# Optimization experiments

Hardware: AMD Instinct MI355X
Metric: run time of the kernel (lower is better)

The kernel has to match this reference:

```python
import jax, jax.numpy as jnp
import numpy as np

HEAD_NUM = 16
KEY_DIM = 64
EMBED = 1024
KV_OUT = HEAD_NUM * KEY_DIM  # 1024


def setup_inputs() -> dict:
    key = jax.random.key(0)
    ks = jax.random.split(key, 11)
    B, L, E = 2, 2048, EMBED
    scale = 0.02
    return {
        "query": jax.random.normal(ks[0], (B, L, E), jnp.float32),
        "key": jax.random.normal(ks[1], (B, L, E), jnp.float32),
        "value": jax.random.normal(ks[2], (B, L, E), jnp.float32),
        "W_Query": jax.random.normal(ks[3], (E, KV_OUT), jnp.float32) * scale,
        "W_Key": jax.random.normal(ks[4], (E, KV_OUT), jnp.float32) * scale,
        "W_Value": jax.random.normal(ks[5], (E, KV_OUT), jnp.float32) * scale,
        "W_Output": jax.random.normal(ks[6], (KV_OUT, E), jnp.float32) * scale,
        "B_Query": jnp.zeros((KV_OUT,), jnp.float32),
        "B_Key": jnp.zeros((KV_OUT,), jnp.float32),
        "B_Value": jnp.zeros((KV_OUT,), jnp.float32),
        "B_Output": jnp.zeros((E,), jnp.float32),
    }


def reference(query, key, value, W_Query, W_Key, W_Value, W_Output,
              B_Query, B_Key, B_Value, B_Output):
    B, Lq, E = query.shape
    Lk = key.shape[1]
    H, D = HEAD_NUM, KEY_DIM
    # QKV projections + bias
    q = query @ W_Query + B_Query            # [B, Lq, H*D]
    k = key @ W_Key + B_Key                  # [B, Lk, H*D]
    v = value @ W_Value + B_Value            # [B, Lk, H*D]
    # tf.split(axis=2) per head == reshape to [B, L, H, D]
    q = q.reshape(B, Lq, H, D)
    k = k.reshape(B, Lk, H, D)
    v = v.reshape(B, Lk, H, D)
    # scaled dot-product attention (no mask, dropout=0)
    scores = jnp.einsum("bqhd,bkhd->bhqk", q, k) / (D ** 0.5)
    probs = jax.nn.softmax(scores, axis=-1)
    out = jnp.einsum("bhqk,bkhd->bqhd", probs, v)  # [B, Lq, H, D]
    out = out.reshape(B, Lq, H * D)
    return out @ W_Output + B_Output
```

## Files before the change

### kernel.cpp

```cpp
#include <hip/hip_runtime.h>

using u16 = unsigned short;
using u32 = unsigned int;

typedef __attribute__((ext_vector_type(8))) short bf16x8;
typedef __attribute__((ext_vector_type(4))) float f32x4;
typedef __attribute__((ext_vector_type(4))) u32 u32x4;
typedef __attribute__((ext_vector_type(2))) u32 u32x2;
typedef __attribute__((ext_vector_type(4))) _Float16 f16x4;

#define MFMA_BF16_K32(a, b, c) __builtin_amdgcn_mfma_f32_16x16x32_bf16((a), (b), (c), 0, 0, 0)
#define MFMA_F16_K16(a, b, c) __builtin_amdgcn_mfma_f32_16x16x16f16((a), (b), (c), 0, 0, 0)

#define QSCALE 0.18033688011112042f

extern "C" __device__ float __ocml_native_exp2_f32(float);

__device__ __forceinline__ u16 f2bf(float f) {
  u32 u = __builtin_bit_cast(u32, f);
  return (u16)((u + 0x7fffu + ((u >> 16) & 1u)) >> 16);
}

__device__ __forceinline__ u32 pk_f16(float a, float b) {
  auto v = __builtin_amdgcn_cvt_pkrtz(a, b);
  return __builtin_bit_cast(u32, v);
}

__device__ __forceinline__ void load_lds16(const void* g, void* l) {
  __builtin_amdgcn_global_load_lds((__attribute__((address_space(1))) void*)g,
                                   (__attribute__((address_space(3))) void*)l,
                                   16, 0, 0);
}

__global__ __launch_bounds__(256) void cvt_all_kernel(
    const float* __restrict__ q, const float* __restrict__ k, const float* __restrict__ v,
    u16* __restrict__ oq, u16* __restrict__ ok, u16* __restrict__ ov,
    const float* __restrict__ w0, const float* __restrict__ w1,
    const float* __restrict__ w2, const float* __restrict__ w3,
    u16* __restrict__ d0, u16* __restrict__ d1,
    u16* __restrict__ d2, u16* __restrict__ d3) {
  const int id = blockIdx.x;
  const int tid = threadIdx.x;
  if (id < 6144) {
    const int z = id >> 11, bx = id & 2047;
    const float* s = z == 0 ? q : z == 1 ? k : v;
    u16* d = z == 0 ? oq : z == 1 ? ok : ov;
    int i = (bx * 256 + tid) * 8;
    f32x4 a = *(const f32x4*)(s + i);
    f32x4 b = *(const f32x4*)(s + i + 4);
    u32x4 o;
    o.x = (u32)f2bf(a.x) | ((u32)f2bf(a.y) << 16);
    o.y = (u32)f2bf(a.z) | ((u32)f2bf(a.w) << 16);
    o.z = (u32)f2bf(b.x) | ((u32)f2bf(b.y) << 16);
    o.w = (u32)f2bf(b.z) | ((u32)f2bf(b.w) << 16);
    *(u32x4*)(d + i) = o;
    return;
  }
  __shared__ float t[64][65];
  const int r0 = id - 6144;
  const int z = r0 >> 8, rr0 = r0 & 255;
  const int bx = rr0 & 15, by = rr0 >> 4;
  const float* src = z == 0 ? w0 : z == 1 ? w1 : z == 2 ? w2 : w3;
  u16* dst = z == 0 ? d0 : z == 1 ? d1 : z == 2 ? d2 : d3;
  const float scale = (z == 0) ? QSCALE : 1.0f;
  const int r = tid >> 4, c4 = (tid & 15) * 4;
#pragma unroll
  for (int i = 0; i < 4; ++i) {
    int row = r + i * 16;
    f32x4 vv = *(const f32x4*)(src + (by * 64 + row) * 1024 + bx * 64 + c4);
    t[row][c4 + 0] = vv.x;
    t[row][c4 + 1] = vv.y;
    t[row][c4 + 2] = vv.z;
    t[row][c4 + 3] = vv.w;
  }
  __syncthreads();
  const int rw = tid >> 2, cc = (tid & 3) * 16;
  alignas(16) u16 tmp[16];
#pragma unroll
  for (int j = 0; j < 16; ++j) tmp[j] = f2bf(t[cc + j][rw] * scale);
  u32x4* outp = (u32x4*)(dst + (bx * 64 + rw) * 1024 + by * 64 + cc);
  outp[0] = *(const u32x4*)&tmp[0];
  outp[1] = *(const u32x4*)&tmp[8];
}

__global__ __launch_bounds__(256) void gemm_qkv_kernel(
    const u16* __restrict__ x0, const u16* __restrict__ x1, const u16* __restrict__ x2,
    const u16* __restrict__ w0, const u16* __restrict__ w1, const u16* __restrict__ w2,
    const float* __restrict__ b0, const float* __restrict__ b1, const float* __restrict__ b2,
    u16* __restrict__ c0, u16* __restrict__ c1, u16* __restrict__ vt) {
  __shared__ u16 As[128 * 64];
  __shared__ u16 Bs[128 * 64];
  const int lid = blockIdx.x;
  const int xcd = lid & 7, rr = lid >> 3;
  const int nb = rr & 7, slot = rr >> 3;
  const int g = slot * 8 + xcd;
  const int z = g >> 5, m_idx = g & 31;
  const u16* A = z == 0 ? x0 : z == 1 ? x1 : x2;
  const u16* Bt = z == 0 ? w0 : z == 1 ? w1 : w2;
  const float* bias = z == 0 ? b0 : z == 1 ? b1 : b2;
  const float bscale = z == 0 ? QSCALE : 1.0f;
  const int tid = threadIdx.x;
  const int wave = tid >> 6, lane = tid & 63;
  const int l16 = lane & 15, quad = lane >> 4;
  const int l7 = l16 & 7;
  const int wm = wave >> 1, wn = wave & 1;
  const int m0 = m_idx * 128, n0 = nb * 128;

  f32x4 acc[4][4];
  const f32x4 zf = {0.f, 0.f, 0.f, 0.f};
#pragma unroll
  for (int i = 0; i < 4; ++i)
#pragma unroll
    for (int j = 0; j < 4; ++j) acc[i][j] = zf;

  for (int kb = 0; kb < 1024; kb += 64) {
#pragma unroll
    for (int t = 0; t < 4; ++t) {
      int c = wave * 256 + t * 64 + lane;
      int row = c >> 3, sc8 = (c & 7) ^ (row & 7);
      load_lds16(A + (m0 + row) * 1024 + kb + sc8 * 8, &As[(wave * 256 + t * 64) * 8]);
    }
#pragma unroll
    for (int t = 0; t < 4; ++t) {
      int c = wave * 256 + t * 64 + lane;
      int row = c >> 3, sc8 = (c & 7) ^ (row & 7);
      load_lds16(Bt + (n0 + row) * 1024 + kb + sc8 * 8, &Bs[(wave * 256 + t * 64) * 8]);
    }
    asm volatile("s_waitcnt vmcnt(0)" ::: "memory");
    __syncthreads();
#pragma unroll
    for (int ks = 0; ks < 2; ++ks) {
      const int sch = (ks * 4 + quad) ^ l7;
      bf16x8 af[4], bfv[4];
#pragma unroll
      for (int mt = 0; mt < 4; ++mt)
        af[mt] = *(const bf16x8*)&As[(wm * 64 + mt * 16 + l16) * 64 + sch * 8];
#pragma unroll
      for (int nt = 0; nt < 4; ++nt)
        bfv[nt] = *(const bf16x8*)&Bs[(wn * 64 + nt * 16 + l16) * 64 + sch * 8];
#pragma unroll
      for (int mt = 0; mt < 4; ++mt)
#pragma unroll
        for (int nt = 0; nt < 4; ++nt) acc[mt][nt] = MFMA_BF16_K32(af[mt], bfv[nt], acc[mt][nt]);
    }
    __syncthreads();
  }

  float bv[4];
#pragma unroll
  for (int nt = 0; nt < 4; ++nt) bv[nt] = bias[n0 + wn * 64 + nt * 16 + l16] * bscale;
  if (z != 2) {
    u16* C = z == 0 ? c0 : c1;
#pragma unroll
    for (int mt = 0; mt < 4; ++mt)
#pragma unroll
      for (int nt = 0; nt < 4; ++nt)
#pragma unroll
        for (int r = 0; r < 4; ++r) {
          int row = m0 + wm * 64 + mt * 16 + quad * 4 + r;
          int col = n0 + wn * 64 + nt * 16 + l16;
          C[row * 1024 + col] = f2bf(acc[mt][nt][r] + bv[nt]);
        }
  } else {
#pragma unroll
    for (int mt = 0; mt < 4; ++mt)
#pragma unroll
      for (int nt = 0; nt < 4; ++nt)
#pragma unroll
        for (int r = 0; r < 4; ++r) {
          int row = m0 + wm * 64 + mt * 16 + quad * 4 + r;
          int col = n0 + wn * 64 + nt * 16 + l16;
          int bb = row >> 11, kv = row & 2047;
          _Float16 hv = (_Float16)(acc[mt][nt][r] + bv[nt]);
          vt[(bb * 1024 + col) * 2048 + kv] = __builtin_bit_cast(u16, hv);
        }
  }
}

__global__ __launch_bounds__(256) void gemm_out_kernel(const u16* __restrict__ A,
                                                       const u16* __restrict__ Bt,
                                                       const float* __restrict__ bias,
                                                       float* __restrict__ C) {
  __shared__ u16 As[64 * 64];
  __shared__ u16 Bs[128 * 64];
  const int lid = blockIdx.x;
  const int xcd = lid & 7, rr = lid >> 3;
  const int nb = rr & 7, slot = rr >> 3;
  const int by = slot * 8 + xcd;
  const int tid = threadIdx.x;
  const int wave = tid >> 6, lane = tid & 63;
  const int l16 = lane & 15, quad = lane >> 4;
  const int l7 = l16 & 7;
  const int m0 = by * 64, n0 = nb * 128;

  f32x4 acc[4][2];
  const f32x4 zf = {0.f, 0.f, 0.f, 0.f};
#pragma unroll
  for (int i = 0; i < 4; ++i)
#pragma unroll
    for (int j = 0; j < 2; ++j) acc[i][j] = zf;

  for (int kb = 0; kb < 1024; kb += 64) {
#pragma unroll
    for (int t = 0; t < 2; ++t) {
      int c = wave * 128 + t * 64 + lane;
      int row = c >> 3, sc8 = (c & 7) ^ (row & 7);
      load_lds16(A + (m0 + row) * 1024 + kb + sc8 * 8, &As[(wave * 128 + t * 64) * 8]);
    }
#pragma unroll
    for (int t = 0; t < 4; ++t) {
      int c = wave * 256 + t * 64 + lane;
      int row = c >> 3, sc8 = (c & 7) ^ (row & 7);
      load_lds16(Bt + (n0 + row) * 1024 + kb + sc8 * 8, &Bs[(wave * 256 + t * 64) * 8]);
    }
    asm volatile("s_waitcnt vmcnt(0)" ::: "memory");
    __syncthreads();
#pragma unroll
    for (int ks = 0; ks < 2; ++ks) {
      const int sch = (ks * 4 + quad) ^ l7;
      bf16x8 af[4], bfv[2];
#pragma unroll
      for (int mt = 0; mt < 4; ++mt)
        af[mt] = *(const bf16x8*)&As[(mt * 16 + l16) * 64 + sch * 8];
#pragma unroll
      for (int nt = 0; nt < 2; ++nt)
        bfv[nt] = *(const bf16x8*)&Bs[(wave * 32 + nt * 16 + l16) * 64 + sch * 8];
#pragma unroll
      for (int mt = 0; mt < 4; ++mt)
#pragma unroll
        for (int nt = 0; nt < 2; ++nt) acc[mt][nt] = MFMA_BF16_K32(af[mt], bfv[nt], acc[mt][nt]);
    }
    __syncthreads();
  }

  float bv[2];
#pragma unroll
  for (int nt = 0; nt < 2; ++nt) bv[nt] = bias[n0 + wave * 32 + nt * 16 + l16];
#pragma unroll
  for (int mt = 0; mt < 4; ++mt)
#pragma unroll
    for (int nt = 0; nt < 2; ++nt)
#pragma unroll
      for (int r = 0; r < 4; ++r) {
        int row = m0 + mt * 16 + quad * 4 + r;
        int col = n0 + wave * 32 + nt * 16 + l16;
        C[row * 1024 + col] = acc[mt][nt][r] + bv[nt];
      }
}

__global__ __launch_bounds__(256, 4) void flash_kernel(const u16* __restrict__ Q,
                                                       const u16* __restrict__ K,
                                                       const u16* __restrict__ Vt,
                                                       u16* __restrict__ O) {
  __shared__ u16 k_lds[128 * 72];
  __shared__ u16 vt_lds[64 * 132];
  const int tid = threadIdx.x;
  const int wave = tid >> 6, lane = tid & 63;
  const int l16 = lane & 15, quad = lane >> 4;
  const int id = blockIdx.x;
  const int xcd = id & 7, slot = id >> 3;
  const int pair = xcd * 4 + (slot & 3);
  const int qb = slot >> 2;
  const int b = pair >> 4, h = pair & 15;
  const u16* Qh = Q + (b * 2048 + qb * 64) * 1024 + h * 64;
  const u16* Kh = K + b * 2048 * 1024 + h * 64;
  const u16* Vh = Vt + pair * 64 * 2048;

  const int k_row[4] = {(0 * 256 + tid) >> 3, (1 * 256 + tid) >> 3,
                        (2 * 256 + tid) >> 3, (3 * 256 + tid) >> 3};
  const int k_c8 = (tid & 7) * 8;
  const int v_d[4] = {(0 * 256 + tid) >> 4, (1 * 256 + tid) >> 4,
                      (2 * 256 + tid) >> 4, (3 * 256 + tid) >> 4};
  const int v_c = (tid & 15) * 8;

  u32x4 kcur[4], vcur[4], knxt[4], vnxt[4];
#pragma unroll
  for (int t = 0; t < 4; ++t) {
    kcur[t] = *(const u32x4*)(Kh + k_row[t] * 1024 + k_c8);
    vcur[t] = *(const u32x4*)(Vh + v_d[t] * 2048 + v_c);
  }

#pragma unroll
  for (int t = 0; t < 2; ++t) {
    int idx = t * 256 + tid, row = idx >> 3, c8 = (idx & 7) * 8;
    *(u32x4*)&k_lds[row * 72 + c8] = *(const u32x4*)(Qh + row * 1024 + c8);
  }
  __syncthreads();
  bf16x8 qf[2];
#pragma unroll
  for (int ks = 0; ks < 2; ++ks)
    qf[ks] = *(const bf16x8*)&k_lds[(wave * 16 + l16) * 72 + ks * 32 + quad * 8];
  __syncthreads();

  f32x4 o_acc[4];
  const f32x4 zf = {0.f, 0.f, 0.f, 0.f};
#pragma unroll
  for (int dt = 0; dt < 4; ++dt) o_acc[dt] = zf;
  float lp = 0.f;

  for (int kb = 0; kb < 16; ++kb) {
#pragma unroll
    for (int t = 0; t < 4; ++t)
      *(u32x4*)&k_lds[k_row[t] * 72 + k_c8] = kcur[t];
#pragma unroll
    for (int t = 0; t < 4; ++t) {
      u32x2 vlo = {vcur[t].x, vcur[t].y}, vhi = {vcur[t].z, vcur[t].w};
      *(u32x2*)&vt_lds[v_d[t] * 132 + v_c] = vlo;
      *(u32x2*)&vt_lds[v_d[t] * 132 + v_c + 4] = vhi;
    }
    if (kb < 15) {
      const int kv1 = (kb + 1) * 128;
#pragma unroll
      for (int t = 0; t < 4; ++t) {
        knxt[t] = *(const u32x4*)(Kh + (kv1 + k_row[t]) * 1024 + k_c8);
        vnxt[t] = *(const u32x4*)(Vh + v_d[t] * 2048 + kv1 + v_c);
      }
    }
    __syncthreads();

#pragma unroll
    for (int chunk = 0; chunk < 8; ++chunk) {
      f32x4 s = zf;
#pragma unroll
      for (int ks = 0; ks < 2; ++ks) {
        bf16x8 kf = *(const bf16x8*)&k_lds[(chunk * 16 + l16) * 72 + ks * 32 + quad * 8];
        s = MFMA_BF16_K32(kf, qf[ks], s);
      }
      float e0 = __ocml_native_exp2_f32(s.x), e1 = __ocml_native_exp2_f32(s.y);
      float e2 = __ocml_native_exp2_f32(s.z), e3 = __ocml_native_exp2_f32(s.w);
      lp += (e0 + e1) + (e2 + e3);
      union { u32 u[2]; f16x4 v; } pk;
      pk.u[0] = pk_f16(e0, e1);
      pk.u[1] = pk_f16(e2, e3);
#pragma unroll
      for (int dt = 0; dt < 4; ++dt) {
        f16x4 vf = *(const f16x4*)&vt_lds[(dt * 16 + l16) * 132 + chunk * 16 + quad * 4];
        o_acc[dt] = MFMA_F16_K16(pk.v, vf, o_acc[dt]);
      }
    }
    __syncthreads();
#pragma unroll
    for (int t = 0; t < 4; ++t) {
      kcur[t] = knxt[t];
      vcur[t] = vnxt[t];
    }
  }

  lp += __shfl_xor(lp, 16);
  lp += __shfl_xor(lp, 32);
#pragma unroll
  for (int r = 0; r < 4; ++r) {
    float inv = 1.0f / __shfl(lp, quad * 4 + r);
    int row = b * 2048 + qb * 64 + wave * 16 + quad * 4 + r;
#pragma unroll
    for (int dt = 0; dt < 4; ++dt)
      O[row * 1024 + h * 64 + dt * 16 + l16] = f2bf(o_acc[dt][r] * inv);
  }
}

extern "C" void kernel_launch(void* const* d_in, const int* in_sizes, int n_in,
                              void* d_out, int out_size, void* d_ws, size_t ws_size,
                              hipStream_t stream) {
  const float* q = (const float*)d_in[0];
  const float* k = (const float*)d_in[1];
  const float* v = (const float*)d_in[2];
  const float* Wq = (const float*)d_in[3];
  const float* Wk = (const float*)d_in[4];
  const float* Wv = (const float*)d_in[5];
  const float* Wo = (const float*)d_in[6];
  const float* Bq = (const float*)d_in[7];
  const float* Bk = (const float*)d_in[8];
  const float* Bv = (const float*)d_in[9];
  const float* Bo = (const float*)d_in[10];
  float* out = (float*)d_out;

  char* w = (char*)d_ws;
  const size_t MB = 1u << 20;
  u16* xq = (u16*)(w + 0 * MB);
  u16* xk = (u16*)(w + 8 * MB);
  u16* xv = (u16*)(w + 16 * MB);
  u16* wqt = (u16*)(w + 24 * MB);
  u16* wkt = (u16*)(w + 26 * MB);
  u16* wvt = (u16*)(w + 28 * MB);
  u16* wot = (u16*)(w + 30 * MB);
  u16* Qp = (u16*)(w + 32 * MB);
  u16* Kp = (u16*)(w + 40 * MB);
  u16* Vtr = (u16*)(w + 48 * MB);
  u16* At = (u16*)(w + 56 * MB);

  cvt_all_kernel<<<dim3(7168), 256, 0, stream>>>(q, k, v, xq, xk, xv,
                                                 Wq, Wk, Wv, Wo, wqt, wkt, wvt, wot);
  gemm_qkv_kernel<<<dim3(768), 256, 0, stream>>>(xq, xk, xv, wqt, wkt, wvt,
                                                 Bq, Bk, Bv, Qp, Kp, Vtr);
  flash_kernel<<<dim3(1024), 256, 0, stream>>>(Qp, Kp, Vtr, At);
  gemm_out_kernel<<<dim3(512), 256, 0, stream>>>(At, wot, Bo, out);
}
```

Baseline: 230.6 us.

## Split flash attention across KV within block, swizzled direct-to-LDS loads, LDS reduction

Reworks the attention kernel so each wave owns all 64 query rows but only a quarter of each 128-key tile, reusing each K/V fragment across four query subtiles. K and V tiles are loaded straight into XOR-swizzled LDS with async global-to-LDS loads instead of the register double-buffer with padded LDS. Partial outputs and row sums are then reduced across waves through LDS, and only wave 0 writes the result. This raises register use (occupancy hint lowered from 4 to 2) and drops the prefetch overlap, so each tile load is now exposed behind a full wait plus barrier.

```diff
diff --git a/kernel.cpp b/kernel.cpp
--- a/kernel.cpp
+++ b/kernel.cpp
@@ -248,15 +248,18 @@
       }
 }
 
-__global__ __launch_bounds__(256, 4) void flash_kernel(const u16* __restrict__ Q,
+__global__ __launch_bounds__(256, 2) void flash_kernel(const u16* __restrict__ Q,
                                                        const u16* __restrict__ K,
                                                        const u16* __restrict__ Vt,
                                                        u16* __restrict__ O) {
-  __shared__ u16 k_lds[128 * 72];
-  __shared__ u16 vt_lds[64 * 132];
+  __shared__ u16 k_lds[128 * 64];
+  __shared__ u16 vt_lds[64 * 128];
+  __shared__ float lred[4][64];
+  __shared__ float lfin[64];
   const int tid = threadIdx.x;
   const int wave = tid >> 6, lane = tid & 63;
   const int l16 = lane & 15, quad = lane >> 4;
+  const int l7 = l16 & 7;
   const int id = blockIdx.x;
   const int xcd = id & 7, slot = id >> 3;
   const int pair = xcd * 4 + (slot & 3);
@@ -266,95 +269,137 @@
   const u16* Kh = K + b * 2048 * 1024 + h * 64;
   const u16* Vh = Vt + pair * 64 * 2048;
 
-  const int k_row[4] = {(0 * 256 + tid) >> 3, (1 * 256 + tid) >> 3,
-                        (2 * 256 + tid) >> 3, (3 * 256 + tid) >> 3};
-  const int k_c8 = (tid & 7) * 8;
-  const int v_d[4] = {(0 * 256 + tid) >> 4, (1 * 256 + tid) >> 4,
-                      (2 * 256 + tid) >> 4, (3 * 256 + tid) >> 4};
-  const int v_c = (tid & 15) * 8;
-
-  u32x4 kcur[4], vcur[4], knxt[4], vnxt[4];
-#pragma unroll
-  for (int t = 0; t < 4; ++t) {
-    kcur[t] = *(const u32x4*)(Kh + k_row[t] * 1024 + k_c8);
-    vcur[t] = *(const u32x4*)(Vh + v_d[t] * 2048 + v_c);
-  }
-
 #pragma unroll
   for (int t = 0; t < 2; ++t) {
-    int idx = t * 256 + tid, row = idx >> 3, c8 = (idx & 7) * 8;
-    *(u32x4*)&k_lds[row * 72 + c8] = *(const u32x4*)(Qh + row * 1024 + c8);
-  }
-  __syncthreads();
-  bf16x8 qf[2];
-#pragma unroll
-  for (int ks = 0; ks < 2; ++ks)
-    qf[ks] = *(const bf16x8*)&k_lds[(wave * 16 + l16) * 72 + ks * 32 + quad * 8];
-  __syncthreads();
-
-  f32x4 o_acc[4];
+    int c = (t * 4 + wave) * 64 + lane;
+    int row = c >> 3, sc8 = (c & 7) ^ (row & 7);
+    load_lds16(Qh + row * 1024 + sc8 * 8, &k_lds[((t * 4 + wave) * 64) * 8]);
+  }
+  asm volatile("s_waitcnt vmcnt(0)" ::: "memory");
+  __syncthreads();
+  bf16x8 qf[4][2];
+#pragma unroll
+  for (int qn = 0; qn < 4; ++qn)
+#pragma unroll
+    for (int ks = 0; ks < 2; ++ks)
+      qf[qn][ks] = *(const bf16x8*)&k_lds[(qn * 16 + l16) * 64 + (((ks * 4 + quad) ^ l7)) * 8];
+  __syncthreads();
+
+  f32x4 o_acc[4][4];
   const f32x4 zf = {0.f, 0.f, 0.f, 0.f};
 #pragma unroll
-  for (int dt = 0; dt < 4; ++dt) o_acc[dt] = zf;
-  float lp = 0.f;
+  for (int qn = 0; qn < 4; ++qn)
+#pragma unroll
+    for (int dt = 0; dt < 4; ++dt) o_acc[qn][dt] = zf;
+  float lp[4] = {0.f, 0.f, 0.f, 0.f};
 
   for (int kb = 0; kb < 16; ++kb) {
-#pragma unroll
-    for (int t = 0; t < 4; ++t)
-      *(u32x4*)&k_lds[k_row[t] * 72 + k_c8] = kcur[t];
+    const int kv0 = kb * 128;
 #pragma unroll
     for (int t = 0; t < 4; ++t) {
-      u32x2 vlo = {vcur[t].x, vcur[t].y}, vhi = {vcur[t].z, vcur[t].w};
-      *(u32x2*)&vt_lds[v_d[t] * 132 + v_c] = vlo;
-      *(u32x2*)&vt_lds[v_d[t] * 132 + v_c + 4] = vhi;
-    }
-    if (kb < 15) {
-      const int kv1 = (kb + 1) * 128;
-#pragma unroll
-      for (int t = 0; t < 4; ++t) {
-        knxt[t] = *(const u32x4*)(Kh + (kv1 + k_row[t]) * 1024 + k_c8);
-        vnxt[t] = *(const u32x4*)(Vh + v_d[t] * 2048 + kv1 + v_c);
+      int c = (t * 4 + wave) * 64 + lane;
+      int row = c >> 3, sc8 = (c & 7) ^ (row & 7);
+      load_lds16(Kh + (kv0 + row) * 1024 + sc8 * 8, &k_lds[((t * 4 + wave) * 64) * 8]);
+    }
+#pragma unroll
+    for (int t = 0; t < 4; ++t) {
+      int c = (t * 4 + wave) * 64 + lane;
+      int d = c >> 4, sc = (c & 15) ^ (d & 15);
+      load_lds16(Vh + d * 2048 + kv0 + sc * 8, &vt_lds[((t * 4 + wave) * 64) * 8]);
+    }
+    asm volatile("s_waitcnt vmcnt(0)" ::: "memory");
+    __syncthreads();
+
+#pragma unroll
+    for (int c2 = 0; c2 < 2; ++c2) {
+      const int chunk = wave * 2 + c2;
+      f32x4 s_acc[4];
+#pragma unroll
+      for (int qn = 0; qn < 4; ++qn) s_acc[qn] = zf;
+#pragma unroll
+      for (int ks = 0; ks < 2; ++ks) {
+        bf16x8 kf = *(const bf16x8*)&k_lds[(chunk * 16 + l16) * 64 + ((ks * 4 + quad) ^ l7) * 8];
+#pragma unroll
+        for (int qn = 0; qn < 4; ++qn) s_acc[qn] = MFMA_BF16_K32(kf, qf[qn][ks], s_acc[qn]);
       }
-    }
-    __syncthreads();
-
-#pragma unroll
-    for (int chunk = 0; chunk < 8; ++chunk) {
-      f32x4 s = zf;
-#pragma unroll
-      for (int ks = 0; ks < 2; ++ks) {
-        bf16x8 kf = *(const bf16x8*)&k_lds[(chunk * 16 + l16) * 72 + ks * 32 + quad * 8];
-        s = MFMA_BF16_K32(kf, qf[ks], s);
+      union { u32 u[2]; f16x4 v; } pkv[4];
+#pragma unroll
+      for (int qn = 0; qn < 4; ++qn) {
+        float e0 = __ocml_native_exp2_f32(s_acc[qn].x);
+        float e1 = __ocml_native_exp2_f32(s_acc[qn].y);
+        float e2 = __ocml_native_exp2_f32(s_acc[qn].z);
+        float e3 = __ocml_native_exp2_f32(s_acc[qn].w);
+        lp[qn] += (e0 + e1) + (e2 + e3);
+        pkv[qn].u[0] = pk_f16(e0, e1);
+        pkv[qn].u[1] = pk_f16(e2, e3);
       }
-      float e0 = __ocml_native_exp2_f32(s.x), e1 = __ocml_native_exp2_f32(s.y);
-      float e2 = __ocml_native_exp2_f32(s.z), e3 = __ocml_native_exp2_f32(s.w);
-      lp += (e0 + e1) + (e2 + e3);
-      union { u32 u[2]; f16x4 v; } pk;
-      pk.u[0] = pk_f16(e0, e1);
-      pk.u[1] = pk_f16(e2, e3);
 #pragma unroll
       for (int dt = 0; dt < 4; ++dt) {
-        f16x4 vf = *(const f16x4*)&vt_lds[(dt * 16 + l16) * 132 + chunk * 16 + quad * 4];
-        o_acc[dt] = MFMA_F16_K16(pk.v, vf, o_acc[dt]);
+        f16x4 vf = *(const f16x4*)&vt_lds[(dt * 16 + l16) * 128 +
+                                          (((chunk * 2 + (quad >> 1)) ^ l16) * 8) + (quad & 1) * 4];
+#pragma unroll
+        for (int qn = 0; qn < 4; ++qn)
+          o_acc[qn][dt] = MFMA_F16_K16(pkv[qn].v, vf, o_acc[qn][dt]);
       }
     }
     __syncthreads();
-#pragma unroll
-    for (int t = 0; t < 4; ++t) {
-      kcur[t] = knxt[t];
-      vcur[t] = vnxt[t];
-    }
-  }
-
-  lp += __shfl_xor(lp, 16);
-  lp += __shfl_xor(lp, 32);
-#pragma unroll
-  for (int r = 0; r < 4; ++r) {
-    float inv = 1.0f / __shfl(lp, quad * 4 + r);
-    int row = b * 2048 + qb * 64 + wave * 16 + quad * 4 + r;
-#pragma unroll
-    for (int dt = 0; dt < 4; ++dt)
-      O[row * 1024 + h * 64 + dt * 16 + l16] = f2bf(o_acc[dt][r] * inv);
+  }
+
+#pragma unroll
+  for (int qn = 0; qn < 4; ++qn) {
+    lp[qn] += __shfl_xor(lp[qn], 16);
+    lp[qn] += __shfl_xor(lp[qn], 32);
+  }
+  if (quad == 0) {
+#pragma unroll
+    for (int qn = 0; qn < 4; ++qn) lred[wave][qn * 16 + l16] = lp[qn];
+  }
+  float* bufA = (float*)k_lds;
+  float* bufB = (float*)vt_lds;
+  if (wave == 1 || wave == 3) {
+    float* buf = (wave == 1) ? bufA : bufB;
+#pragma unroll
+    for (int qm = 0; qm < 4; ++qm)
+#pragma unroll
+      for (int dt = 0; dt < 4; ++dt)
+        *(f32x4*)&buf[(((qm * 4 + dt) * 4 + quad) * 16 + l16) * 4] = o_acc[qm][dt];
+  }
+  __syncthreads();
+  if (tid < 64) lfin[tid] = lred[0][tid] + lred[1][tid] + lred[2][tid] + lred[3][tid];
+  if (wave == 0 || wave == 2) {
+    float* buf = (wave == 0) ? bufA : bufB;
+#pragma unroll
+    for (int qm = 0; qm < 4; ++qm)
+#pragma unroll
+      for (int dt = 0; dt < 4; ++dt)
+        o_acc[qm][dt] += *(const f32x4*)&buf[(((qm * 4 + dt) * 4 + quad) * 16 + l16) * 4];
+  }
+  __syncthreads();
+  if (wave == 2) {
+#pragma unroll
+    for (int qm = 0; qm < 4; ++qm)
+#pragma unroll
+      for (int dt = 0; dt < 4; ++dt)
+        *(f32x4*)&bufA[(((qm * 4 + dt) * 4 + quad) * 16 + l16) * 4] = o_acc[qm][dt];
+  }
+  __syncthreads();
+  if (wave == 0) {
+#pragma unroll
+    for (int qm = 0; qm < 4; ++qm)
+#pragma unroll
+      for (int dt = 0; dt < 4; ++dt)
+        o_acc[qm][dt] += *(const f32x4*)&bufA[(((qm * 4 + dt) * 4 + quad) * 16 + l16) * 4];
+#pragma unroll
+    for (int qm = 0; qm < 4; ++qm)
+#pragma unroll
+      for (int r = 0; r < 4; ++r) {
+        int qrow = qm * 16 + quad * 4 + r;
+        float inv = 1.0f / lfin[qrow];
+        int row = b * 2048 + qb * 64 + qrow;
+#pragma unroll
+        for (int dt = 0; dt < 4; ++dt)
+          O[row * 1024 + h * 64 + dt * 16 + l16] = f2bf(o_acc[qm][dt][r] * inv);
+      }
   }
 }
 
```

New measurement: 227.4 us. No clear change (-1.4%).
